# Kernel tuning notes

Hardware: AMD Instinct MI355X
Metric: run time of the kernel (lower is better)

The kernel has to match this reference:

```python
import jax, jax.numpy as jnp
import numpy as np

B, K, C = 1024, 8, 10   # predicted points, concepts, classes per concept
N = 8192                # background (training) set size
EPS = 1e-13


def setup_inputs() -> dict:
    key = jax.random.key(0)
    k1, k2, k3 = jax.random.split(key, 3)
    c_p = jax.random.normal(k1, (B, K, C), dtype=jnp.float32)
    bandwidth = jnp.ones((K * C,), dtype=jnp.float32)  # learned param, init 1.0
    c_in = jax.random.randint(k2, (N, K), 0, C, dtype=jnp.int64)
    delta_in = jax.random.randint(k3, (N,), 0, 2, dtype=jnp.int32)
    return {"c_p": c_p, "bandwidth": bandwidth, "c_in": c_in, "delta_in": delta_in}


def _beran(c_p, bandwidth, c_in, delta_in):
    # ---- GaussKernel l2 metric ----
    proba = jax.nn.softmax(c_p, axis=-1)                      # [B,K,C]
    bw = jnp.clip(bandwidth, 0.001, 10.0).reshape(K, C)       # [K,C]
    onehot = jax.nn.one_hot(c_in, C, dtype=proba.dtype)       # [N,K,C]
    # sum((p - l)^2 / bw) = sum(p^2/bw) - 2 sum(p*l/bw) + sum(l^2/bw)
    A = jnp.sum(proba * proba / bw, axis=(1, 2))              # [B]
    D = jnp.einsum('nkc,kc->n', onehot, 1.0 / bw)             # [N]
    cross = jnp.einsum('bkc,nkc->bn', proba / bw, onehot)     # [B,N]
    metric = A[:, None] - 2.0 * cross + D[None, :]            # [B,N]
    weights = jnp.exp(-metric)
    s = jnp.sum(weights, axis=1, keepdims=True)               # normalize over background axis
    bad = s < EPS
    W = jnp.where(bad, 0.0, weights / jnp.where(bad, 1.0, s)) # [B,N]

    # ---- Beran cumulative hazard scan ----
    w_cumsum = jnp.cumsum(W, axis=1)
    shifted = w_cumsum - W
    ones = jnp.ones_like(shifted)
    bad2 = jnp.isclose(shifted, ones) | jnp.isclose(w_cumsum, ones)
    shifted = jnp.where(bad2, 0.0, shifted)
    w_cumsum = jnp.where(bad2, 0.0, w_cumsum)
    xi = jnp.log(1.0 - shifted) - jnp.log(1.0 - w_cumsum)
    filtered_xi = delta_in.astype(xi.dtype)[None, :] * xi
    hazards = jnp.cumsum(filtered_xi, axis=1)
    surv_func = jnp.exp(-hazards)                             # [B,N]
    first_step = 1.0 - surv_func[:, :1]
    surv_steps = jnp.concatenate([first_step, surv_func[:, :-1] - surv_func[:, 1:]], axis=1)
    ss = jnp.sum(surv_steps, axis=1, keepdims=True)
    bad3 = ss < EPS
    surv_steps = jnp.where(bad3, 0.0, surv_steps / jnp.where(bad3, 1.0, ss))
    return surv_func, surv_steps


def reference(c_p, bandwidth, c_in, delta_in):
    return _beran(c_p, bandwidth, c_in, delta_in)
```

## Files before the change

kernel.cpp:

```cpp
#include <hip/hip_runtime.h>

#define NN 8192
#define BB 1024
#define KK 8
#define CC 10
#define NT 512
#define CHUNK (NN/NT)
#define NW (NT/64)

__device__ __forceinline__ int swz(int n) {
    return (n & ~31) | ((n + (n >> 5)) & 31);
}

__global__ void pack_kernel(const int* __restrict__ c_in, const int* __restrict__ delta_in,
                            unsigned* __restrict__ pairs, unsigned* __restrict__ dmask_g) {
    int n = blockIdx.x * blockDim.x + threadIdx.x;
    if (n >= NN) return;
    const int4* p = reinterpret_cast<const int4*>(c_in + (size_t)n * KK);
    int4 lo = p[0], hi = p[1];
    unsigned p0 = (unsigned)(lo.x * 10 + lo.y);
    unsigned p1 = (unsigned)(lo.z * 10 + lo.w);
    unsigned p2 = (unsigned)(hi.x * 10 + hi.y);
    unsigned p3 = (unsigned)(hi.z * 10 + hi.w);
    pairs[n] = p0 | (p1 << 7) | (p2 << 14) | (p3 << 21);
    unsigned long long bal = __ballot(delta_in[n] & 1);
    if ((threadIdx.x & 63) == 0) {
        dmask_g[n >> 5]       = (unsigned)(bal & 0xffffffffull);
        dmask_g[(n >> 5) + 1] = (unsigned)(bal >> 32);
    }
}

__device__ __forceinline__ float block_excl_scan(float v, int lane, int wv, float* ws) {
    float x = v;
    #pragma unroll
    for (int d = 1; d < 64; d <<= 1) {
        float y = __shfl_up(x, d);
        if (lane >= d) x += y;
    }
    if (lane == 63) ws[wv] = x;
    __syncthreads();
    float woff = 0.0f;
    #pragma unroll
    for (int w = 0; w < NW - 1; w++)
        if (w < wv) woff += ws[w];
    return woff + (x - v);
}

__global__ __launch_bounds__(NT, 8) void beran_kernel(
    const float* __restrict__ c_p, const float* __restrict__ bandwidth,
    const int* __restrict__ c_in, const int* __restrict__ delta_in,
    const unsigned* __restrict__ pairs, const unsigned* __restrict__ dmask_g,
    float* __restrict__ out)
{
    __shared__ float a[NN];
    __shared__ float ttab[KK * CC];
    __shared__ float ttab2[4 * 100];
    __shared__ float Apart[KK];
    __shared__ float wsumS[NW];
    __shared__ float wsumB[NW];
    __shared__ float wsumC[NW];
    __shared__ unsigned dmls[NN / 32];

    const int b    = blockIdx.x;
    const int t    = threadIdx.x;
    const int lane = t & 63;
    const int wv   = t >> 6;
    const int base = t * CHUNK;

    if (t < KK) {
        const int k = t;
        float v[CC];
        float mx = -1e30f;
        #pragma unroll
        for (int c = 0; c < CC; c++) { v[c] = c_p[((size_t)b*KK + k)*CC + c]; mx = fmaxf(mx, v[c]); }
        float se = 0.0f;
        #pragma unroll
        for (int c = 0; c < CC; c++) { v[c] = __expf(v[c] - mx); se += v[c]; }
        float inv = 1.0f / se;
        float Ak = 0.0f;
        #pragma unroll
        for (int c = 0; c < CC; c++) {
            float p  = v[c] * inv;
            float bw = bandwidth[k*CC + c];
            bw = fminf(fmaxf(bw, 0.001f), 10.0f);
            float ib = 1.0f / bw;
            ttab[k*CC + c] = ib - 2.0f * p * ib;
            Ak += p * p * ib;
        }
        Apart[k] = Ak;
    }
    __syncthreads();
    if (t < 400) {
        int k = t / 100, p = t % 100;
        ttab2[t] = ttab[(k*2)*CC + p/10] + ttab[(k*2+1)*CC + p%10];
    }
    float A = 0.0f;
    #pragma unroll
    for (int k = 0; k < KK; k++) A += Apart[k];
    __syncthreads();

    float lsum = 0.0f;
    unsigned dm;
    if (pairs) {
        for (int j = 0; j < CHUNK; j++) {
            int n = j * NT + t;
            unsigned pk = pairs[n];
            float m = A;
            m += ttab2[pk & 127];
            m += ttab2[100 + ((pk >> 7) & 127)];
            m += ttab2[200 + ((pk >> 14) & 127)];
            m += ttab2[300 + (pk >> 21)];
            float w = __expf(-m);
            a[swz(n)] = w;
            lsum += w;
        }
    } else {
        for (int j = 0; j < CHUNK; j++) {
            int n = j * NT + t;
            unsigned long long bal = __ballot(delta_in[n] & 1);
            if (lane == 0) {
                dmls[(n >> 5)]     = (unsigned)(bal & 0xffffffffull);
                dmls[(n >> 5) + 1] = (unsigned)(bal >> 32);
            }
            const int4* p4 = reinterpret_cast<const int4*>(c_in + (size_t)n * KK);
            int4 lo4 = p4[0], hi4 = p4[1];
            float m = A;
            m += ttab[0*CC + lo4.x] + ttab[1*CC + lo4.y] + ttab[2*CC + lo4.z] + ttab[3*CC + lo4.w];
            m += ttab[4*CC + hi4.x] + ttab[5*CC + hi4.y] + ttab[6*CC + hi4.z] + ttab[7*CC + hi4.w];
            float w = __expf(-m);
            a[swz(n)] = w;
            lsum += w;
        }
    }

    float wsr = lsum;
    #pragma unroll
    for (int d = 32; d; d >>= 1) wsr += __shfl_xor(wsr, d);
    if (lane == 0) wsumS[wv] = wsr;
    __syncthreads();
    float s = 0.0f;
    #pragma unroll
    for (int w = 0; w < NW; w++) s += wsumS[w];
    const float invs = (s < 1e-13f) ? 0.0f : 1.0f / s;
    {
        unsigned dm32 = pairs ? dmask_g[t >> 1] : dmls[t >> 1];
        dm = (dm32 >> ((t & 1) * 16)) & 0xffffu;
    }

    float creg[CHUNK];
    float run = 0.0f;
    #pragma unroll
    for (int i = 0; i < CHUNK; i++) { run += a[swz(base + i)]; creg[i] = run; }
    const float off_raw = block_excl_scan(run, lane, wv, wsumB);

    const float ISO = 1.00001e-5f;
    float csprev = off_raw * invs;
    float Lprev  = __logf(1.0f - csprev);
    float run2 = 0.0f;
    #pragma unroll
    for (int i = 0; i < CHUNK; i++) {
        float cs = (creg[i] + off_raw) * invs;
        float L  = __logf(1.0f - cs);
        bool bad = (fabsf(csprev - 1.0f) <= ISO) || (fabsf(cs - 1.0f) <= ISO);
        float xi = bad ? 0.0f : (Lprev - L);
        float f  = ((dm >> i) & 1u) ? xi : 0.0f;
        run2 += f;
        creg[i] = run2;
        csprev = cs;
        Lprev  = L;
    }
    const float off2 = block_excl_scan(run2, lane, wv, wsumC);

    #pragma unroll
    for (int i = 0; i < CHUNK; i++) a[swz(base + i)] = __expf(-(creg[i] + off2));
    __syncthreads();

    const float surv_last = a[swz(NN - 1)];
    const float ss = 1.0f - surv_last;
    const float invss = (ss < 1e-13f) ? 0.0f : 1.0f / ss;
    float* outS = out + (size_t)b * NN;
    float* outT = out + (size_t)BB * NN + (size_t)b * NN;
    #pragma unroll
    for (int j = 0; j < NN / (NT * 4); j++) {
        int n0 = j * NT * 4 + t * 4;
        float s0 = a[swz(n0)];
        float s1 = a[swz(n0 + 1)];
        float s2 = a[swz(n0 + 2)];
        float s3 = a[swz(n0 + 3)];
        float sp = (n0 == 0) ? 1.0f : a[swz(n0 - 1)];
        float4 sv = make_float4(s0, s1, s2, s3);
        *reinterpret_cast<float4*>(outS + n0) = sv;
        float4 st = make_float4((sp - s0) * invss, (s0 - s1) * invss,
                                (s1 - s2) * invss, (s2 - s3) * invss);
        *reinterpret_cast<float4*>(outT + n0) = st;
    }
}

extern "C" void kernel_launch(void* const* d_in, const int* in_sizes, int n_in,
                              void* d_out, int out_size, void* d_ws, size_t ws_size,
                              hipStream_t stream) {
    const float* c_p       = (const float*)d_in[0];
    const float* bandwidth = (const float*)d_in[1];
    const int*   c_in      = (const int*)d_in[2];
    const int*   delta_in  = (const int*)d_in[3];
    float* out = (float*)d_out;

    unsigned* pairs   = nullptr;
    unsigned* dmask_g = nullptr;
    const size_t need = (size_t)NN * sizeof(unsigned) + (size_t)(NN / 32) * sizeof(unsigned);
    if (ws_size >= need) {
        pairs   = (unsigned*)d_ws;
        dmask_g = (unsigned*)((char*)d_ws + (size_t)NN * sizeof(unsigned));
        pack_kernel<<<NN / 256, 256, 0, stream>>>(c_in, delta_in, pairs, dmask_g);
    }
    beran_kernel<<<BB, NT, 0, stream>>>(c_p, bandwidth, c_in, delta_in, pairs, dmask_g, out);
}
```

Before: 30.23 us.

## Keep per-thread chunk in registers, drop shared staging array

Each thread now computes weights for its contiguous chunk directly into registers via vectorized pair loads, so the 32KB shared array and its swizzled writes and reads go away. The weight total comes out of the first block scan, and the normalizer uses the last hazard total instead of reading the final element. Outputs are written straight from registers, with each thread writing its own contiguous 64-byte span. This frees LDS and removes barriers, but global stores are now strided per thread instead of coalesced across lanes.

```diff
diff --git a/kernel.cpp b/kernel.cpp
--- a/kernel.cpp
+++ b/kernel.cpp
@@ -7,10 +7,6 @@
 #define NT 512
 #define CHUNK (NN/NT)
 #define NW (NT/64)
-
-__device__ __forceinline__ int swz(int n) {
-    return (n & ~31) | ((n + (n >> 5)) & 31);
-}
 
 __global__ void pack_kernel(const int* __restrict__ c_in, const int* __restrict__ delta_in,
                             unsigned* __restrict__ pairs, unsigned* __restrict__ dmask_g) {
@@ -30,7 +26,8 @@
     }
 }
 
-__device__ __forceinline__ float block_excl_scan(float v, int lane, int wv, float* ws) {
+__device__ __forceinline__ float block_excl_scan(float v, int lane, int wv, float* ws,
+                                                 float* total) {
     float x = v;
     #pragma unroll
     for (int d = 1; d < 64; d <<= 1) {
@@ -39,11 +36,15 @@
     }
     if (lane == 63) ws[wv] = x;
     __syncthreads();
-    float woff = 0.0f;
+    float off = x - v, tot = 0.0f;
     #pragma unroll
-    for (int w = 0; w < NW - 1; w++)
-        if (w < wv) woff += ws[w];
-    return woff + (x - v);
+    for (int w = 0; w < NW; w++) {
+        float y = ws[w];
+        tot += y;
+        if (w < wv) off += y;
+    }
+    *total = tot;
+    return off;
 }
 
 __global__ __launch_bounds__(NT, 8) void beran_kernel(
@@ -52,14 +53,11 @@
     const unsigned* __restrict__ pairs, const unsigned* __restrict__ dmask_g,
     float* __restrict__ out)
 {
-    __shared__ float a[NN];
     __shared__ float ttab[KK * CC];
     __shared__ float ttab2[4 * 100];
     __shared__ float Apart[KK];
-    __shared__ float wsumS[NW];
-    __shared__ float wsumB[NW];
-    __shared__ float wsumC[NW];
-    __shared__ unsigned dmls[NN / 32];
+    __shared__ float wsB[NW];
+    __shared__ float wsC[NW];
 
     const int b    = blockIdx.x;
     const int t    = threadIdx.x;
@@ -99,59 +97,44 @@
     for (int k = 0; k < KK; k++) A += Apart[k];
     __syncthreads();
 
-    float lsum = 0.0f;
-    unsigned dm;
+    float creg[CHUNK];
+    unsigned dm = 0;
+    float run = 0.0f;
     if (pairs) {
-        for (int j = 0; j < CHUNK; j++) {
-            int n = j * NT + t;
-            unsigned pk = pairs[n];
-            float m = A;
-            m += ttab2[pk & 127];
-            m += ttab2[100 + ((pk >> 7) & 127)];
-            m += ttab2[200 + ((pk >> 14) & 127)];
-            m += ttab2[300 + (pk >> 21)];
-            float w = __expf(-m);
-            a[swz(n)] = w;
-            lsum += w;
+        {
+            unsigned dm32 = dmask_g[t >> 1];
+            dm = (dm32 >> ((t & 1) * 16)) & 0xffffu;
+        }
+        #pragma unroll
+        for (int g = 0; g < CHUNK / 4; g++) {
+            uint4 pk = *reinterpret_cast<const uint4*>(pairs + base + g * 4);
+#define DOPAIR(pw, idx) { \
+            float m = A + ttab2[(pw) & 127] + ttab2[100 + (((pw) >> 7) & 127)] \
+                    + ttab2[200 + (((pw) >> 14) & 127)] + ttab2[300 + ((pw) >> 21)]; \
+            run += __expf(-m); creg[idx] = run; }
+            DOPAIR(pk.x, g*4 + 0)
+            DOPAIR(pk.y, g*4 + 1)
+            DOPAIR(pk.z, g*4 + 2)
+            DOPAIR(pk.w, g*4 + 3)
+#undef DOPAIR
         }
     } else {
-        for (int j = 0; j < CHUNK; j++) {
-            int n = j * NT + t;
-            unsigned long long bal = __ballot(delta_in[n] & 1);
-            if (lane == 0) {
-                dmls[(n >> 5)]     = (unsigned)(bal & 0xffffffffull);
-                dmls[(n >> 5) + 1] = (unsigned)(bal >> 32);
-            }
-            const int4* p4 = reinterpret_cast<const int4*>(c_in + (size_t)n * KK);
+        #pragma unroll
+        for (int i = 0; i < CHUNK; i++) {
+            const int4* p4 = reinterpret_cast<const int4*>(c_in + (size_t)(base + i) * KK);
             int4 lo4 = p4[0], hi4 = p4[1];
             float m = A;
             m += ttab[0*CC + lo4.x] + ttab[1*CC + lo4.y] + ttab[2*CC + lo4.z] + ttab[3*CC + lo4.w];
             m += ttab[4*CC + hi4.x] + ttab[5*CC + hi4.y] + ttab[6*CC + hi4.z] + ttab[7*CC + hi4.w];
-            float w = __expf(-m);
-            a[swz(n)] = w;
-            lsum += w;
+            run += __expf(-m);
+            creg[i] = run;
+            dm |= (unsigned)(delta_in[base + i] & 1) << i;
         }
     }
 
-    float wsr = lsum;
-    #pragma unroll
-    for (int d = 32; d; d >>= 1) wsr += __shfl_xor(wsr, d);
-    if (lane == 0) wsumS[wv] = wsr;
-    __syncthreads();
-    float s = 0.0f;
-    #pragma unroll
-    for (int w = 0; w < NW; w++) s += wsumS[w];
+    float s;
+    const float off_raw = block_excl_scan(run, lane, wv, wsB, &s);
     const float invs = (s < 1e-13f) ? 0.0f : 1.0f / s;
-    {
-        unsigned dm32 = pairs ? dmask_g[t >> 1] : dmls[t >> 1];
-        dm = (dm32 >> ((t & 1) * 16)) & 0xffffu;
-    }
-
-    float creg[CHUNK];
-    float run = 0.0f;
-    #pragma unroll
-    for (int i = 0; i < CHUNK; i++) { run += a[swz(base + i)]; creg[i] = run; }
-    const float off_raw = block_excl_scan(run, lane, wv, wsumB);
 
     const float ISO = 1.00001e-5f;
     float csprev = off_raw * invs;
@@ -169,30 +152,26 @@
         csprev = cs;
         Lprev  = L;
     }
-    const float off2 = block_excl_scan(run2, lane, wv, wsumC);
 
+    float H;
+    const float off2 = block_excl_scan(run2, lane, wv, wsC, &H);
+
+    const float ss = 1.0f - __expf(-H);
+    const float invss = (ss < 1e-13f) ? 0.0f : 1.0f / ss;
+    float sprev = (t == 0) ? 1.0f : __expf(-off2);
+    float* outS = out + (size_t)b * NN + base;
+    float* outT = out + (size_t)BB * NN + (size_t)b * NN + base;
     #pragma unroll
-    for (int i = 0; i < CHUNK; i++) a[swz(base + i)] = __expf(-(creg[i] + off2));
-    __syncthreads();
-
-    const float surv_last = a[swz(NN - 1)];
-    const float ss = 1.0f - surv_last;
-    const float invss = (ss < 1e-13f) ? 0.0f : 1.0f / ss;
-    float* outS = out + (size_t)b * NN;
-    float* outT = out + (size_t)BB * NN + (size_t)b * NN;
-    #pragma unroll
-    for (int j = 0; j < NN / (NT * 4); j++) {
-        int n0 = j * NT * 4 + t * 4;
-        float s0 = a[swz(n0)];
-        float s1 = a[swz(n0 + 1)];
-        float s2 = a[swz(n0 + 2)];
-        float s3 = a[swz(n0 + 3)];
-        float sp = (n0 == 0) ? 1.0f : a[swz(n0 - 1)];
-        float4 sv = make_float4(s0, s1, s2, s3);
-        *reinterpret_cast<float4*>(outS + n0) = sv;
-        float4 st = make_float4((sp - s0) * invss, (s0 - s1) * invss,
-                                (s1 - s2) * invss, (s2 - s3) * invss);
-        *reinterpret_cast<float4*>(outT + n0) = st;
+    for (int g = 0; g < CHUNK / 4; g++) {
+        float s0 = __expf(-(creg[g*4 + 0] + off2));
+        float s1 = __expf(-(creg[g*4 + 1] + off2));
+        float s2 = __expf(-(creg[g*4 + 2] + off2));
+        float s3 = __expf(-(creg[g*4 + 3] + off2));
+        *reinterpret_cast<float4*>(outS + g*4) = make_float4(s0, s1, s2, s3);
+        *reinterpret_cast<float4*>(outT + g*4) =
+            make_float4((sprev - s0) * invss, (s0 - s1) * invss,
+                        (s1 - s2) * invss, (s2 - s3) * invss);
+        sprev = s3;
     }
 }
 
```

After: 38.09 us. +26.0%, slower.
